# Performance work log

Measured on AMD Instinct MI355X. Metric: run time of the kernel, lower is better.

The kernel has to match this reference:

```python
import jax, jax.numpy as jnp
import numpy as np

NUM_ELEMENTS = 14
FLUID_ELEMS = (0, 3, 4, 10, 11)  # empty, water, gas, lava, acid
B, C, H, W = 16, 20, 512, 512


def setup_inputs() -> dict:
    key = jax.random.key(0)
    ks = jax.random.split(key, 6)
    # world: element one-hot channels + density + gravity + momentum + velocity + extra
    elem_ids = jax.random.randint(ks[0], (B, H, W), 0, NUM_ELEMENTS)
    onehot = jax.nn.one_hot(elem_ids, NUM_ELEMENTS, dtype=jnp.float32)  # [B,H,W,NE]
    onehot = jnp.transpose(onehot, (0, 3, 1, 2))
    density = jax.random.uniform(ks[1], (B, 1, H, W), dtype=jnp.float32) * 4.0
    gravity = (jax.random.uniform(ks[2], (B, 1, H, W)) > 0.2).astype(jnp.float32)
    rest = jax.random.normal(ks[3], (B, C - NUM_ELEMENTS - 2, H, W), dtype=jnp.float32)
    world = jnp.concatenate([onehot, density, gravity, rest], axis=1)
    rk = jax.random.split(ks[4], 4)
    return {
        "world": world,
        "rand_movement": jax.random.uniform(rk[0], (B, 1, H, W), dtype=jnp.float32),
        "rand_interact": jax.random.uniform(rk[1], (B, 1, H, W), dtype=jnp.float32),
        "rand_element": jax.random.uniform(rk[2], (B, 1, H, W), dtype=jnp.float32),
        "velocity_field": jax.random.normal(rk[3], (B, 2, H, W), dtype=jnp.float32),
        "did_gravity": jax.random.normal(ks[5], (B, 1, H, W), dtype=jnp.float32),
    }


def _fluid_flow(world, rand_movement, did_gravity):
    dens_c, grav_c, fm_c = NUM_ELEMENTS, NUM_ELEMENTS + 1, NUM_ELEMENTS + 2
    new_fm = jnp.zeros_like(world[:, :1])
    not_did_gravity = did_gravity <= 0
    for elem in FLUID_ELEMS:
        for fall_left in (True, False):
            sh = 1 if fall_left else -1
            gdir = lambda x, s=sh: jnp.roll(x, s, axis=3)      # toward fall direction
            gnot = lambda x, s=sh: jnp.roll(x, -s, axis=3)     # opposite direction
            # momentum channel is a live view of world in the torch code -> re-read
            fall_dir = (rand_movement + world[:, fm_c:fm_c + 1] + new_fm) > 0.5
            is_element = world[:, elem:elem + 1] == 1
            is_right_element = gnot(is_element)
            density = world[:, dens_c:dens_c + 1]
            is_matching_fall = fall_dir if fall_left else ~fall_dir
            is_right_matching_fall = gnot(is_matching_fall)
            is_left_density_lower = (density - gdir(density)) > 0
            is_right_density_higher = (gnot(density) - density) > 0
            is_gravity = world[:, grav_c:grav_c + 1] == 1
            is_left_gravity = gdir(is_gravity) & is_gravity
            is_right_gravity = gnot(is_gravity) & is_gravity
            becomes_left = (is_matching_fall & is_element & not_did_gravity
                            & is_left_density_lower & is_left_gravity)
            becomes_right = (is_right_matching_fall & is_right_element & gnot(not_did_gravity)
                             & is_right_density_higher & is_right_gravity)
            new_fm = new_fm + becomes_right.astype(world.dtype) * (2.0 if fall_left else -2.0)
            a = becomes_left.astype(world.dtype)
            b = becomes_right.astype(world.dtype)
            # interp2: (~a & ~b)*world + a*world_left + b*world_right
            world = (1.0 - a) * (1.0 - b) * world + a * gdir(world) + b * gnot(world)
    world = world.at[:, fm_c:fm_c + 1].set(new_fm)
    return world


def reference(world, rand_movement, rand_interact, rand_element, velocity_field, did_gravity):
    world = _fluid_flow(world, rand_movement, did_gravity)
    return (world, rand_movement, rand_interact, rand_element, velocity_field, did_gravity)
```

## Files before the change

kernel.cpp:

```cpp
#include <hip/hip_runtime.h>


#define CCH 20
#define BHW ((size_t)4194304)
#define CH  ((size_t)262144)

#define LD8(dst, p) { const float4* _q=(const float4*)(p); float4 _x=_q[0],_y=_q[1]; \
  dst[0]=_x.x;dst[1]=_x.y;dst[2]=_x.z;dst[3]=_x.w;dst[4]=_y.x;dst[5]=_y.y;dst[6]=_y.z;dst[7]=_y.w; }
#define ST8(p, v) { float4* _q=(float4*)(p); _q[0]=make_float4(v[0],v[1],v[2],v[3]); \
  _q[1]=make_float4(v[4],v[5],v[6],v[7]); }

__global__ __launch_bounds__(256) void fluid_wave_kernel(
    const float* __restrict__ world_in,
    const float* __restrict__ rm_in,
    const float* __restrict__ ri_in,
    const float* __restrict__ re_in,
    const float* __restrict__ vf_in,
    const float* __restrict__ dg_in,
    float* __restrict__ out)
{
    __shared__ float s_g[4][2][528];

    const int lane = threadIdx.x & 63;
    const int wv   = threadIdx.x >> 6;
    const int row  = (blockIdx.x << 2) + wv;
    const int b    = row >> 9;
    const int h    = row & 511;
    const int px0  = lane << 3;

    const size_t srow  = (size_t)row * 512;
    const size_t wrow  = (((size_t)b * CCH) * 512 + h) * 512;
    const size_t vrow0 = (((size_t)b * 2) * 512 + h) * 512;
    const size_t vrow1 = vrow0 + CH;

    const float* win  = world_in + wrow;
    float*       wout = out + wrow;

    float t[8];
    LD8(t, ri_in + srow + px0);  ST8(out + 21*BHW + srow + px0, t);
    LD8(t, re_in + srow + px0);  ST8(out + 22*BHW + srow + px0, t);
    LD8(t, vf_in + vrow0 + px0); ST8(out + 23*BHW + vrow0 + px0, t);
    LD8(t, vf_in + vrow1 + px0); ST8(out + 23*BHW + vrow1 + px0, t);

    float rm[8], dgv[8], dens[8], fm[8], nf[8];
    uint32_t code[8], sA[8], sB[8];
    LD8(rm,  rm_in + srow + px0);  ST8(out + 20*BHW + srow + px0, rm);
    LD8(dgv, dg_in + srow + px0);  ST8(out + 25*BHW + srow + px0, dgv);
    LD8(dens, win + 14*CH + px0);
    LD8(fm,   win + 16*CH + px0);

    uint32_t ndgm = 0;
    #pragma unroll
    for (int j = 0; j < 8; ++j) ndgm |= (uint32_t)(dgv[j] <= 0.0f) << j;

    LD8(t, win + 15*CH + px0);
    #pragma unroll
    for (int j = 0; j < 8; ++j) code[j] = (uint32_t)(t[j] == 1.0f) << 20;
    LD8(t, win +  0*CH + px0);
    #pragma unroll
    for (int j = 0; j < 8; ++j) code[j] |= (uint32_t)(t[j] == 1.0f);
    LD8(t, win +  3*CH + px0);
    #pragma unroll
    for (int j = 0; j < 8; ++j) code[j] |= (uint32_t)(t[j] == 1.0f) << 4;
    LD8(t, win +  4*CH + px0);
    #pragma unroll
    for (int j = 0; j < 8; ++j) code[j] |= (uint32_t)(t[j] == 1.0f) << 8;
    LD8(t, win + 10*CH + px0);
    #pragma unroll
    for (int j = 0; j < 8; ++j) code[j] |= (uint32_t)(t[j] == 1.0f) << 12;
    LD8(t, win + 11*CH + px0);
    #pragma unroll
    for (int j = 0; j < 8; ++j) code[j] |= (uint32_t)(t[j] == 1.0f) << 16;

    float cur[8], nxt[8], nx2[8];
    LD8(cur, win + 1*CH + px0);

    #pragma unroll
    for (int j = 0; j < 8; ++j) {
        sA[j] = 1u | ((uint32_t)(px0 + j) << 4);
        sB[j] = 0u;
        nf[j] = 0.0f;
    }

    const int lft = (lane + 63) & 63, rgt = (lane + 1) & 63;

    #pragma unroll 1
    for (int ei = 0; ei < 5; ++ei) {
        if (ei == 2) { LD8(nxt, win + 2*CH + px0); }
        if (ei == 4) { LD8(nx2, win + 5*CH + px0); }

        const int sft = ei * 4;
        #pragma unroll
        for (int fi = 0; fi < 2; ++fi) {
            const bool  fl = (fi == 0);
            const float k  = fl ? 2.0f : -2.0f;

            const float dL = __shfl(dens[7], lft), dR = __shfl(dens[0], rgt);
            const float fL = __shfl(fm[7],  lft), fR = __shfl(fm[0],  rgt);
            const uint32_t cL = (uint32_t)__shfl((int)code[7], lft);
            const uint32_t cR = (uint32_t)__shfl((int)code[0], rgt);
            const uint32_t AL = (uint32_t)__shfl((int)sA[7], lft);
            const uint32_t AR = (uint32_t)__shfl((int)sA[0], rgt);
            const uint32_t BL = (uint32_t)__shfl((int)sB[7], lft);
            const uint32_t BR = (uint32_t)__shfl((int)sB[0], rgt);

            uint32_t am = 0;
            #pragma unroll
            for (int j = 0; j < 8; ++j) {
                float dwm; uint32_t cwm;
                if (fl) { dwm = j ? dens[j-1] : dL;       cwm = j ? code[j-1] : cL; }
                else    { dwm = (j<7) ? dens[j+1] : dR;   cwm = (j<7) ? code[j+1] : cR; }
                const bool fd  = ((rm[j] + fm[j]) + nf[j]) > 0.5f;
                const bool imf = fl ? fd : !fd;
                const bool a = imf
                    && (((code[j] >> sft) & 15u) == 1u)
                    && (((ndgm >> j) & 1u) != 0u)
                    && ((dens[j] - dwm) > 0.0f)
                    && (((cwm    >> 20) & 15u) == 1u)
                    && (((code[j] >> 20) & 15u) == 1u);
                am |= (uint32_t)a << j;
            }

            const uint32_t aLm = (uint32_t)__shfl((int)am, lft);
            const uint32_t aRm = (uint32_t)__shfl((int)am, rgt);
            const uint32_t bm = fl ? ((am >> 1) | ((aRm & 1u) << 7))
                                   : (((am << 1) & 0xFFu) | ((aLm >> 7) & 1u));

            float prD = dL, prF = fL;
            uint32_t prC = cL, prA = AL, prB = BL;
            #pragma unroll
            for (int j = 0; j < 8; ++j) {
                const float    ahD = (j<7) ? dens[j+1] : dR;
                const float    ahF = (j<7) ? fm[j+1]   : fR;
                const uint32_t ahC = (j<7) ? code[j+1] : cR;
                const uint32_t ahA = (j<7) ? sA[j+1]   : AR;
                const uint32_t ahB = (j<7) ? sB[j+1]   : BR;
                const float    wmD = fl ? prD : ahD, wpD = fl ? ahD : prD;
                const float    wmF = fl ? prF : ahF, wpF = fl ? ahF : prF;
                const uint32_t wmC = fl ? prC : ahC, wpC = fl ? ahC : prC;
                const uint32_t wmA = fl ? prA : ahA, wpA = fl ? ahA : prA;
                const uint32_t wmB = fl ? prB : ahB, wpB = fl ? ahB : prB;
                const bool a  = (am >> j) & 1u;
                const bool bb = (bm >> j) & 1u;
                if (bb) nf[j] += k;
                prD = dens[j]; prF = fm[j]; prC = code[j]; prA = sA[j]; prB = sB[j];
                if (a & bb) {
                    dens[j] = wmD + wpD; fm[j] = wmF + wpF; code[j] = wmC + wpC;
                    const uint32_t c1 = wmA & 15u, c2 = wpA & 15u;
                    const uint64_t l1 = ((uint64_t)(wmA >> 4)) | ((uint64_t)wmB << 27);
                    const uint64_t l2 = ((uint64_t)(wpA >> 4)) | ((uint64_t)wpB << 27);
                    uint32_t cnt = c1 + c2; if (cnt > 6u) cnt = 6u;
                    const uint64_t all = l1 | (l2 << (9u * c1));
                    sA[j] = cnt | ((uint32_t)(all & 0x7FFFFFFull) << 4);
                    sB[j] = (uint32_t)((all >> 27) & 0x7FFFFFFull);
                } else if (a) {
                    dens[j] = wmD; fm[j] = wmF; code[j] = wmC; sA[j] = wmA; sB[j] = wmB;
                } else if (bb) {
                    dens[j] = wpD; fm[j] = wpF; code[j] = wpC; sA[j] = wpA; sB[j] = wpB;
                }
            }
        }
    }

    float o[8];
    #pragma unroll
    for (int j=0;j<8;++j) o[j] = (float)( code[j]        & 15u); ST8(wout +  0*CH + px0, o);
    #pragma unroll
    for (int j=0;j<8;++j) o[j] = (float)((code[j] >>  4) & 15u); ST8(wout +  3*CH + px0, o);
    #pragma unroll
    for (int j=0;j<8;++j) o[j] = (float)((code[j] >>  8) & 15u); ST8(wout +  4*CH + px0, o);
    #pragma unroll
    for (int j=0;j<8;++j) o[j] = (float)((code[j] >> 12) & 15u); ST8(wout + 10*CH + px0, o);
    #pragma unroll
    for (int j=0;j<8;++j) o[j] = (float)((code[j] >> 16) & 15u); ST8(wout + 11*CH + px0, o);
    #pragma unroll
    for (int j=0;j<8;++j) o[j] = (float)((code[j] >> 20) & 15u); ST8(wout + 15*CH + px0, o);
    ST8(wout + 14*CH + px0, dens);
    ST8(wout + 16*CH + px0, nf);

    uint32_t multi = 0;
    int sidx0[8];
    #pragma unroll
    for (int j = 0; j < 8; ++j) {
        const uint32_t p = (sA[j] >> 4) & 511u;
        sidx0[j] = (int)(p + (p >> 5));
        multi |= (uint32_t)((sA[j] & 15u) > 1u) << j;
    }
    const int pad = lane >> 2;

    static const int GCv[12] = {1,2,5,6,7,8,9,12,13,17,18,19};
    float nx3[8];
    #pragma unroll
    for (int g = 0; g < 12; ++g) {
        if (g < 9) { LD8(nx3, win + (size_t)GCv[g + 3] * CH + px0); }
        float* buf = &s_g[wv][g & 1][0];
        #pragma unroll
        for (int j = 0; j < 8; ++j) buf[px0 + pad + j] = cur[j];
        float v[8];
        #pragma unroll
        for (int j = 0; j < 8; ++j) v[j] = buf[sidx0[j]];
        if (multi) {
            #pragma unroll
            for (int j = 0; j < 8; ++j) if ((multi >> j) & 1u) {
                const uint32_t A = sA[j], c = A & 15u, Bv = sB[j];
                uint32_t p1 = (A >> 13) & 511u; float x = v[j] + buf[p1 + (p1 >> 5)];
                if (c > 2u) { uint32_t p2 = (A >> 22) & 511u; x += buf[p2 + (p2 >> 5)];
                  if (c > 3u) { uint32_t p3 = Bv & 511u; x += buf[p3 + (p3 >> 5)];
                    if (c > 4u) { uint32_t p4 = (Bv >> 9) & 511u; x += buf[p4 + (p4 >> 5)];
                      if (c > 5u) { uint32_t p5 = (Bv >> 18) & 511u; x += buf[p5 + (p5 >> 5)]; } } } }
                v[j] = x;
            }
        }
        ST8(wout + (size_t)GCv[g] * CH + px0, v);
        #pragma unroll
        for (int j = 0; j < 8; ++j) { cur[j] = nxt[j]; nxt[j] = nx2[j]; nx2[j] = nx3[j]; }
    }
}

extern "C" void kernel_launch(void* const* d_in, const int* in_sizes, int n_in,
                              void* d_out, int out_size, void* d_ws, size_t ws_size,
                              hipStream_t stream) {
    const float* world = (const float*)d_in[0];
    const float* rm    = (const float*)d_in[1];
    const float* ri    = (const float*)d_in[2];
    const float* re    = (const float*)d_in[3];
    const float* vf    = (const float*)d_in[4];
    const float* dg    = (const float*)d_in[5];
    float* out = (float*)d_out;

    dim3 grid(2048), block(256);
    fluid_wave_kernel<<<grid, block, 0, stream>>>(world, rm, ri, re, vf, dg, out);
}
```

Baseline: 182.1 us.

## Split passthrough copies into dedicated copy blocks interleaved with fluid blocks

The grid becomes 3072 blocks, and every third block does only a flat float4 copy of rand_interact, rand_element and velocity_field into the output. The other blocks compute the fluid step without those copies. The prefetch depth of the gather loop is also cut from three rows ahead to one, which lowers register pressure but exposes more load latency. The aim is to balance memory-bound copy work against the compute-heavier fluid blocks and to raise occupancy.

```diff
diff --git a/kernel.cpp b/kernel.cpp
--- a/kernel.cpp
+++ b/kernel.cpp
@@ -10,7 +10,7 @@
 #define ST8(p, v) { float4* _q=(float4*)(p); _q[0]=make_float4(v[0],v[1],v[2],v[3]); \
   _q[1]=make_float4(v[4],v[5],v[6],v[7]); }
 
-__global__ __launch_bounds__(256) void fluid_wave_kernel(
+__global__ __launch_bounds__(256) void fluid_mix_kernel(
     const float* __restrict__ world_in,
     const float* __restrict__ rm_in,
     const float* __restrict__ ri_in,
@@ -21,27 +21,39 @@
 {
     __shared__ float s_g[4][2][528];
 
-    const int lane = threadIdx.x & 63;
-    const int wv   = threadIdx.x >> 6;
-    const int row  = (blockIdx.x << 2) + wv;
+    const int tid = threadIdx.x;
+    const int bi  = blockIdx.x;
+
+    if (bi % 3 == 2) {
+        const int cid = bi / 3;
+        const float* srcs[3] = { ri_in, re_in, vf_in };
+        const size_t dst0[3] = { 21*BHW, 22*BHW, 23*BHW };
+        const size_t lens[3] = { 1048576, 1048576, 2097152 };
+        #pragma unroll
+        for (int it = 0; it < 16; ++it) {
+            size_t q = (size_t)cid * 4096 + (size_t)it * 256 + tid;
+            int s = 0;
+            while (q >= lens[s]) { q -= lens[s]; ++s; }
+            ((float4*)(out + dst0[s]))[q] = ((const float4*)srcs[s])[q];
+        }
+        return;
+    }
+
+    const int fid  = (bi / 3) * 2 + (bi % 3);
+    const int lane = tid & 63;
+    const int wv   = tid >> 6;
+    const int row  = (fid << 2) + wv;
     const int b    = row >> 9;
     const int h    = row & 511;
     const int px0  = lane << 3;
 
-    const size_t srow  = (size_t)row * 512;
-    const size_t wrow  = (((size_t)b * CCH) * 512 + h) * 512;
-    const size_t vrow0 = (((size_t)b * 2) * 512 + h) * 512;
-    const size_t vrow1 = vrow0 + CH;
+    const size_t srow = (size_t)row * 512;
+    const size_t wrow = (((size_t)b * CCH) * 512 + h) * 512;
 
     const float* win  = world_in + wrow;
     float*       wout = out + wrow;
 
     float t[8];
-    LD8(t, ri_in + srow + px0);  ST8(out + 21*BHW + srow + px0, t);
-    LD8(t, re_in + srow + px0);  ST8(out + 22*BHW + srow + px0, t);
-    LD8(t, vf_in + vrow0 + px0); ST8(out + 23*BHW + vrow0 + px0, t);
-    LD8(t, vf_in + vrow1 + px0); ST8(out + 23*BHW + vrow1 + px0, t);
-
     float rm[8], dgv[8], dens[8], fm[8], nf[8];
     uint32_t code[8], sA[8], sB[8];
     LD8(rm,  rm_in + srow + px0);  ST8(out + 20*BHW + srow + px0, rm);
@@ -72,7 +84,7 @@
     #pragma unroll
     for (int j = 0; j < 8; ++j) code[j] |= (uint32_t)(t[j] == 1.0f) << 16;
 
-    float cur[8], nxt[8], nx2[8];
+    float cur[8];
     LD8(cur, win + 1*CH + px0);
 
     #pragma unroll
@@ -86,9 +98,6 @@
 
     #pragma unroll 1
     for (int ei = 0; ei < 5; ++ei) {
-        if (ei == 2) { LD8(nxt, win + 2*CH + px0); }
-        if (ei == 4) { LD8(nx2, win + 5*CH + px0); }
-
         const int sft = ei * 4;
         #pragma unroll
         for (int fi = 0; fi < 2; ++fi) {
@@ -189,13 +198,13 @@
     const int pad = lane >> 2;
 
     static const int GCv[12] = {1,2,5,6,7,8,9,12,13,17,18,19};
-    float nx3[8];
+    float nxt[8];
     #pragma unroll
     for (int g = 0; g < 12; ++g) {
-        if (g < 9) { LD8(nx3, win + (size_t)GCv[g + 3] * CH + px0); }
         float* buf = &s_g[wv][g & 1][0];
         #pragma unroll
         for (int j = 0; j < 8; ++j) buf[px0 + pad + j] = cur[j];
+        if (g < 11) { LD8(nxt, win + (size_t)GCv[g + 1] * CH + px0); }
         float v[8];
         #pragma unroll
         for (int j = 0; j < 8; ++j) v[j] = buf[sidx0[j]];
@@ -213,7 +222,7 @@
         }
         ST8(wout + (size_t)GCv[g] * CH + px0, v);
         #pragma unroll
-        for (int j = 0; j < 8; ++j) { cur[j] = nxt[j]; nxt[j] = nx2[j]; nx2[j] = nx3[j]; }
+        for (int j = 0; j < 8; ++j) cur[j] = nxt[j];
     }
 }
 
@@ -228,6 +237,6 @@
     const float* dg    = (const float*)d_in[5];
     float* out = (float*)d_out;
 
-    dim3 grid(2048), block(256);
-    fluid_wave_kernel<<<grid, block, 0, stream>>>(world, rm, ri, re, vf, dg, out);
+    dim3 grid(3072), block(256);
+    fluid_mix_kernel<<<grid, block, 0, stream>>>(world, rm, ri, re, vf, dg, out);
 }
```

Result: slower. 193.9 us (+6.5%).
